# Kernel optimization log

Hardware: AMD Instinct MI355X
Metric: run time of the kernel (lower is better)

Reference implementation:

```python
import jax, jax.numpy as jnp
import numpy as np

B, N, D = 4, 4096, 1024
H, DH = 16, 64
EPS = 1e-5


def setup_inputs() -> dict:
    key = jax.random.key(0)
    ks = jax.random.split(key, 4)
    x = jax.random.normal(ks[0], (B, N, D), dtype=jnp.float32)
    w_qkv = jax.random.normal(ks[1], (D, 3 * H * DH), dtype=jnp.float32) * 0.02
    # per-head LayerNorm affine params (one LayerNorm(dim_head) per head)
    gamma_k = jnp.ones((H, DH), dtype=jnp.float32)
    beta_k = jnp.zeros((H, DH), dtype=jnp.float32)
    gamma_v = jnp.ones((H, DH), dtype=jnp.float32)
    beta_v = jnp.zeros((H, DH), dtype=jnp.float32)
    w_out = jax.random.normal(ks[2], (H * DH, D), dtype=jnp.float32) * 0.02
    b_out = jnp.zeros((D,), dtype=jnp.float32)
    return {"x": x, "w_qkv": w_qkv, "gamma_k": gamma_k, "beta_k": beta_k,
            "gamma_v": gamma_v, "beta_v": beta_v, "w_out": w_out, "b_out": b_out}


def _per_head_layernorm(t, gamma, beta):
    # t: [b, h, n, d]; gamma/beta: [h, d] (distinct affine per head)
    mu = jnp.mean(t, axis=-1, keepdims=True)
    var = jnp.mean(jnp.square(t - mu), axis=-1, keepdims=True)  # biased, as torch LayerNorm
    tn = (t - mu) * jax.lax.rsqrt(var + EPS)
    return tn * gamma[None, :, None, :] + beta[None, :, None, :]


def reference(x, w_qkv, gamma_k, beta_k, gamma_v, beta_v, w_out, b_out):
    b, n, _ = x.shape
    h, dh = gamma_k.shape
    qkv = jnp.einsum('bnd,de->bne', x, w_qkv)  # [b, n, 3*h*dh]
    q, k, v = jnp.split(qkv, 3, axis=-1)

    def to_heads(t):  # b n (h d) -> b h n d
        return t.reshape(b, n, h, dh).transpose(0, 2, 1, 3)

    q, k, v = to_heads(q), to_heads(k), to_heads(v)
    k = _per_head_layernorm(k, gamma_k, beta_k)
    v = _per_head_layernorm(v, gamma_v, beta_v)
    # linear attention: scores = k^T v / n  -> [b, h, d, d]
    scores = jnp.einsum('bhnd,bhne->bhde', k, v) / n
    out = jnp.einsum('bhnd,bhde->bhne', q, scores)  # [b, h, n, d]
    out = out.transpose(0, 2, 1, 3).reshape(b, n, h * dh)
    return jnp.einsum('bne,ed->bnd', out, w_out) + b_out
```

## Files before the change

kernel.cpp:

```cpp
#include <hip/hip_runtime.h>

typedef __attribute__((ext_vector_type(4))) float f32x4;
typedef __attribute__((ext_vector_type(8))) short s16x8;

#define DEV static __device__ __forceinline__

typedef __attribute__((address_space(3))) void lds_t;
typedef __attribute__((address_space(1))) void gbl_t;

DEV void gload_lds16(const void* g, void* l) {
    __builtin_amdgcn_global_load_lds((gbl_t*)g, (lds_t*)l, 16, 0, 0);
}

DEV ushort f2bf(float f) {
    unsigned u = __float_as_uint(f);
    u += 0x7fffu + ((u >> 16) & 1u);
    return (ushort)(u >> 16);
}
DEV float bf2f(ushort h) { return __uint_as_float(((unsigned)h) << 16); }

#define FULLBAR() do {                              \
    __builtin_amdgcn_sched_barrier(0);              \
    asm volatile("" ::: "memory");                  \
    __builtin_amdgcn_s_barrier();                   \
    asm volatile("" ::: "memory");                  \
    __builtin_amdgcn_sched_barrier(0);              \
} while (0)

#define WAITVM(n) asm volatile("s_waitcnt vmcnt(" #n ")" ::: "memory")
#define LGKM0() asm volatile("s_waitcnt lgkmcnt(0)" ::: "memory")

__global__ void pack_x_k(const float* __restrict__ x, ushort* __restrict__ xb, int n4) {
    int stride = gridDim.x * blockDim.x;
    for (int i = blockIdx.x * blockDim.x + threadIdx.x; i < n4; i += stride) {
        float4 v = reinterpret_cast<const float4*>(x)[i];
        ushort4 o;
        o.x = f2bf(v.x); o.y = f2bf(v.y); o.z = f2bf(v.z); o.w = f2bf(v.w);
        reinterpret_cast<ushort4*>(xb)[i] = o;
    }
}

__global__ void pack_wq_k(const float* __restrict__ w, ushort* __restrict__ o) {
    int i = blockIdx.x * 256 + threadIdx.x;
    int r = i >> 8, c4 = i & 255;
    float4 v = *reinterpret_cast<const float4*>(w + (size_t)r * 3072 + c4 * 4);
    ushort4 u;
    u.x = f2bf(v.x); u.y = f2bf(v.y); u.z = f2bf(v.z); u.w = f2bf(v.w);
    *reinterpret_cast<ushort4*>(o + (size_t)r * 1024 + c4 * 4) = u;
}

__global__ void trans_pack_k(const float* __restrict__ in, ushort* __restrict__ out,
                             int R, int C, int col0) {
    __shared__ float tile[32][33];
    int bx = col0 + blockIdx.x * 32, by = blockIdx.y * 32;
    int tx = threadIdx.x, ty = threadIdx.y;
#pragma unroll
    for (int i = 0; i < 32; i += 8)
        tile[ty + i][tx] = in[(size_t)(by + ty + i) * C + bx + tx];
    __syncthreads();
#pragma unroll
    for (int i = 0; i < 32; i += 8)
        out[(size_t)(bx - col0 + ty + i) * R + by + tx] = f2bf(tile[tx][ty + i]);
}

template <int MODE>
__global__ __launch_bounds__(512, 1) void gemm_bt_k(
    const ushort* __restrict__ A, const ushort* __restrict__ Bt,
    int Nn, int col0, size_t b_stride,
    ushort* __restrict__ ko, ushort* __restrict__ vo,
    const float* __restrict__ gk, const float* __restrict__ bk,
    const float* __restrict__ gv, const float* __restrict__ bv,
    const float* __restrict__ bias, float* __restrict__ outf)
{
    __shared__ __align__(16) ushort SH[65536];
    const int t = threadIdx.x;
    const int w = t >> 6, lane = t & 63;
    const int wr = w >> 2, wc = w & 3;
    const int lrow = lane & 15, kh = lane >> 4;

    int bid = blockIdx.y * gridDim.x + blockIdx.x;
    int C8 = (gridDim.x * gridDim.y) >> 3;
    int nid = (bid & 7) * C8 + (bid >> 3);
    int n0 = (nid % gridDim.x) * 256;
    int m0 = (nid / gridDim.x) * 256;

    const ushort* Bte = (MODE == 1) ? Bt + (size_t)(m0 >> 12) * b_stride : Bt;

    const int srow8 = w * 8 + (lane >> 3);
    const int scol = ((lane & 7) ^ ((lane >> 3) & 7)) * 8;

    const int g0 = ((kh) ^ (lrow & 7)) * 8;
    const int g1 = ((4 + kh) ^ (lrow & 7)) * 8;

    f32x4 acc[8][4] = {};
    s16x8 bfr[4][2];
    s16x8 af[8];

    auto STAGE_A = [&](int kt, int s, int h) {
        ushort* As = SH + s * 32768;
        const ushort* Ag = A + (size_t)(m0 + h * 128 + srow8) * 1024 + kt * 64 + scol;
        gload_lds16(Ag,                     As + (h * 128 + w * 8) * 64);
        gload_lds16(Ag + (size_t)64 * 1024, As + (h * 128 + 64 + w * 8) * 64);
    };
    auto STAGE_B = [&](int kt, int s, int h) {
        ushort* Bs = SH + s * 32768 + 16384;
        const ushort* Bg = Bte + (size_t)(n0 + h * 128 + srow8) * 1024 + kt * 64 + scol;
        gload_lds16(Bg,                     Bs + (h * 128 + w * 8) * 64);
        gload_lds16(Bg + (size_t)64 * 1024, Bs + (h * 128 + 64 + w * 8) * 64);
    };

    STAGE_A(0, 0, 0); STAGE_A(0, 0, 1);
    STAGE_B(0, 0, 0); STAGE_B(0, 0, 1);
    STAGE_B(1, 1, 0); STAGE_B(1, 1, 1);

    for (int kt = 0; kt < 16; ++kt) {
        const int p = kt & 1, q = p ^ 1;
        const ushort* As = SH + p * 32768;
        const ushort* Bs = As + 16384;

        if (kt < 15) { WAITVM(4); } else { WAITVM(0); }
        FULLBAR();

#pragma unroll
        for (int ni = 0; ni < 4; ni++) {
            const int r = (wc * 64 + ni * 16 + lrow) * 64;
            bfr[ni][0] = *reinterpret_cast<const s16x8*>(&Bs[r + g0]);
            bfr[ni][1] = *reinterpret_cast<const s16x8*>(&Bs[r + g1]);
        }
#pragma unroll
        for (int mi = 0; mi < 8; mi++)
            af[mi] = *reinterpret_cast<const s16x8*>(&As[(wr * 128 + mi * 16 + lrow) * 64 + g0]);
        if (kt + 1 < 16) { STAGE_A(kt + 1, q, 0); STAGE_A(kt + 1, q, 1); }

        __builtin_amdgcn_s_setprio(1);
#pragma unroll
        for (int mi = 0; mi < 8; mi++)
#pragma unroll
            for (int ni = 0; ni < 4; ni++)
                acc[mi][ni] = __builtin_amdgcn_mfma_f32_16x16x32_bf16(af[mi], bfr[ni][0], acc[mi][ni], 0, 0, 0);
        __builtin_amdgcn_s_setprio(0);

        LGKM0();
        FULLBAR();

        if (kt + 2 < 16) { STAGE_B(kt + 2, p, 0); STAGE_B(kt + 2, p, 1); }
#pragma unroll
        for (int mi = 0; mi < 8; mi++)
            af[mi] = *reinterpret_cast<const s16x8*>(&As[(wr * 128 + mi * 16 + lrow) * 64 + g1]);

        __builtin_amdgcn_s_setprio(1);
#pragma unroll
        for (int mi = 0; mi < 8; mi++)
#pragma unroll
            for (int ni = 0; ni < 4; ni++)
                acc[mi][ni] = __builtin_amdgcn_mfma_f32_16x16x32_bf16(af[mi], bfr[ni][1], acc[mi][ni], 0, 0, 0);
        __builtin_amdgcn_s_setprio(0);
    }

    if (MODE == 0) {
        const int e0 = col0 + n0 + wc * 64;
        const int which = e0 >> 10;
        const int h = (e0 >> 6) & 15;
        const float* g  = (which == 1) ? gk : gv;
        const float* bb = (which == 1) ? bk : bv;
        ushort* dst     = (which == 1) ? ko : vo;
        float gr[4], br[4];
#pragma unroll
        for (int ni = 0; ni < 4; ni++) {
            gr[ni] = g[h * 64 + ni * 16 + lrow];
            br[ni] = bb[h * 64 + ni * 16 + lrow];
        }
        __syncthreads();
        ushort* Tl = SH + w * 4608;
#pragma unroll
        for (int chunk = 0; chunk < 2; ++chunk) {
#pragma unroll
            for (int mi2 = 0; mi2 < 4; ++mi2) {
                const int mi = chunk * 4 + mi2;
#pragma unroll
                for (int j = 0; j < 4; j++) {
                    float s = acc[mi][0][j] + acc[mi][1][j] + acc[mi][2][j] + acc[mi][3][j];
                    s += __shfl_xor(s, 1, 64);
                    s += __shfl_xor(s, 2, 64);
                    s += __shfl_xor(s, 4, 64);
                    s += __shfl_xor(s, 8, 64);
                    float mu = s * (1.f / 64.f);
                    float t2 = 0.f;
#pragma unroll
                    for (int ni = 0; ni < 4; ni++) {
                        float dd = acc[mi][ni][j] - mu;
                        t2 += dd * dd;
                    }
                    t2 += __shfl_xor(t2, 1, 64);
                    t2 += __shfl_xor(t2, 2, 64);
                    t2 += __shfl_xor(t2, 4, 64);
                    t2 += __shfl_xor(t2, 8, 64);
                    float inv = rsqrtf(t2 * (1.f / 64.f) + 1e-5f);
#pragma unroll
                    for (int ni = 0; ni < 4; ni++) {
                        float y = (acc[mi][ni][j] - mu) * inv * gr[ni] + br[ni];
                        Tl[(ni * 16 + lrow) * 72 + mi2 * 16 + kh * 4 + j] = f2bf(y);
                    }
                }
            }
            const int mrow0 = m0 + wr * 128 + chunk * 64;
            const int b = mrow0 >> 12, ns0 = mrow0 & 4095;
            ushort* obase = dst + (((size_t)b * 16 + h) * 64) * 4096 + ns0;
#pragma unroll
            for (int p2 = 0; p2 < 8; ++p2) {
                int d = p2 * 8 + (lane >> 3);
                int mo = (lane & 7) * 8;
                s16x8 vv = *reinterpret_cast<const s16x8*>(&Tl[d * 72 + mo]);
                *reinterpret_cast<s16x8*>(obase + (size_t)d * 4096 + mo) = vv;
            }
        }
    } else {
#pragma unroll
        for (int mi = 0; mi < 8; mi++)
#pragma unroll
            for (int ni = 0; ni < 4; ni++) {
                int e = n0 + wc * 64 + ni * 16 + lrow;
                float bv2 = bias[e];
#pragma unroll
                for (int j = 0; j < 4; j++) {
                    int m = m0 + wr * 128 + mi * 16 + kh * 4 + j;
                    outf[(size_t)m * Nn + e] = acc[mi][ni][j] + bv2;
                }
            }
    }
}

__global__ __launch_bounds__(256) void fold_k(const ushort* __restrict__ A,
                                              const ushort* __restrict__ Bt,
                                              ushort* __restrict__ out)
{
    __shared__ __align__(16) ushort SH2[24576];
    const int t = threadIdx.x;
    const int w = t >> 6, lane = t & 63;
    const int wm = w >> 1, wn = w & 1;
    const int lrow = lane & 15, kh = lane >> 4;
    const int n0 = blockIdx.x * 128, m0 = blockIdx.y * 128;

    const int srow0 = w * 32 + (lane >> 2);
    const int scolSwz = (((lane & 3) ^ ((lane >> 3) & 3)) * 8);

    f32x4 acc[4][4] = {};

    auto STAGE = [&](int kt, int s) {
        ushort* As = SH2 + s * 8192;
        ushort* Bs = As + 4096;
        const ushort* Ag = A  + (size_t)(m0 + srow0) * 1024 + kt * 32 + scolSwz;
        const ushort* Bg = Bt + (size_t)(n0 + srow0) * 1024 + kt * 32 + scolSwz;
        gload_lds16(Ag,             As + w * 1024);
        gload_lds16(Bg,             Bs + w * 1024);
        gload_lds16(Ag + 16 * 1024, As + w * 1024 + 512);
        gload_lds16(Bg + 16 * 1024, Bs + w * 1024 + 512);
    };

    const int rdoff = (kh ^ ((lrow >> 1) & 3)) * 8;

    auto COMPUTE = [&](int s) {
        const ushort* As = SH2 + s * 8192;
        const ushort* Bs = As + 4096;
        s16x8 af[4], bfr[4];
#pragma unroll
        for (int mi = 0; mi < 4; mi++)
            af[mi] = *reinterpret_cast<const s16x8*>(&As[(wm * 64 + mi * 16 + lrow) * 32 + rdoff]);
#pragma unroll
        for (int ni = 0; ni < 4; ni++)
            bfr[ni] = *reinterpret_cast<const s16x8*>(&Bs[(wn * 64 + ni * 16 + lrow) * 32 + rdoff]);
#pragma unroll
        for (int mi = 0; mi < 4; mi++)
#pragma unroll
            for (int ni = 0; ni < 4; ni++)
                acc[mi][ni] = __builtin_amdgcn_mfma_f32_16x16x32_bf16(af[mi], bfr[ni], acc[mi][ni], 0, 0, 0);
    };

    STAGE(0, 0);
    STAGE(1, 1);
    int ss = 2, sc_ = 0;
    for (int kt = 0; kt < 30; ++kt) {
        STAGE(kt + 2, ss);
        ss = (ss == 2) ? 0 : ss + 1;
        WAITVM(8);
        FULLBAR();
        COMPUTE(sc_);
        sc_ = (sc_ == 2) ? 0 : sc_ + 1;
        FULLBAR();
    }
    WAITVM(4); FULLBAR(); COMPUTE(0); FULLBAR();
    WAITVM(0); FULLBAR(); COMPUTE(1);

#pragma unroll
    for (int mi = 0; mi < 4; mi++)
#pragma unroll
        for (int ni = 0; ni < 4; ni++) {
            int e = n0 + wn * 64 + ni * 16 + lrow;
#pragma unroll
            for (int j = 0; j < 4; j++) {
                int m = m0 + wm * 64 + mi * 16 + kh * 4 + j;
                out[(size_t)m * 1024 + e] = f2bf(acc[mi][ni][j]);
            }
        }
}

__global__ __launch_bounds__(256) void scores_k(const ushort* __restrict__ kT,
                                                const ushort* __restrict__ vT,
                                                float* __restrict__ sc)
{
    __shared__ float red[4][64][65];
    const int bh = blockIdx.y;
    const int t = threadIdx.x;
    const int w = t >> 6, lane = t & 63;
    const int lrow = lane & 15, kh = lane >> 4;
    const ushort* ka = kT + (size_t)bh * 64 * 4096;
    const ushort* va = vT + (size_t)bh * 64 * 4096;
    const int n0 = blockIdx.x * 512 + w * 128;

    f32x4 acc[4][4] = {};
#pragma unroll
    for (int ks = 0; ks < 4; ++ks) {
        const int n = n0 + ks * 32 + kh * 8;
        s16x8 af[4], bfr[4];
#pragma unroll
        for (int mi = 0; mi < 4; mi++)
            af[mi] = *reinterpret_cast<const s16x8*>(ka + (size_t)(mi * 16 + lrow) * 4096 + n);
#pragma unroll
        for (int ni = 0; ni < 4; ni++)
            bfr[ni] = *reinterpret_cast<const s16x8*>(va + (size_t)(ni * 16 + lrow) * 4096 + n);
#pragma unroll
        for (int mi = 0; mi < 4; mi++)
#pragma unroll
            for (int ni = 0; ni < 4; ni++)
                acc[mi][ni] = __builtin_amdgcn_mfma_f32_16x16x32_bf16(af[mi], bfr[ni], acc[mi][ni], 0, 0, 0);
    }
#pragma unroll
    for (int mi = 0; mi < 4; mi++)
#pragma unroll
        for (int ni = 0; ni < 4; ni++)
#pragma unroll
            for (int j = 0; j < 4; j++)
                red[w][mi * 16 + kh * 4 + j][ni * 16 + lrow] = acc[mi][ni][j];
    __syncthreads();
    const float scale = 1.f / 4096.f;
    for (int idx = t; idx < 4096; idx += 256) {
        int d = idx >> 6, e = idx & 63;
        float s = red[0][d][e] + red[1][d][e] + red[2][d][e] + red[3][d][e];
        atomicAdd(&sc[(size_t)bh * 4096 + idx], s * scale);
    }
}

__global__ __launch_bounds__(256) void wprime_k(const float* __restrict__ sc,
                                                const ushort* __restrict__ woutT,
                                                ushort* __restrict__ wpT)
{
    __shared__ float scl[64][65];
    __shared__ ushort wl[128][72];
    int bh = blockIdx.y;
    int b = bh >> 4, h = bh & 15;
    int f0 = blockIdx.x * 128;
    int t = threadIdx.x;
    for (int i = t; i < 4096; i += 256) {
        int d2 = i >> 6, e = i & 63;
        scl[e][d2] = sc[(size_t)bh * 4096 + i];
    }
    for (int i = t; i < 1024; i += 256) {
        int fl = i >> 3, c = i & 7;
        *reinterpret_cast<int4*>(&wl[fl][c * 8]) =
            *reinterpret_cast<const int4*>(woutT + (size_t)(f0 + fl) * 1024 + h * 64 + c * 8);
    }
    __syncthreads();
    int dd = (t & 7) * 8;
    int fl0 = t >> 3;
#pragma unroll
    for (int fi = 0; fi < 4; ++fi) {
        int fl = fi * 32 + fl0;
        float acc[8] = {};
        for (int e = 0; e < 64; ++e) {
            float wv = bf2f(wl[fl][e]);
#pragma unroll
            for (int i = 0; i < 8; ++i)
                acc[i] = fmaf(wv, scl[e][dd + i], acc[i]);
        }
        ushort4 o0, o1;
        o0.x = f2bf(acc[0]); o0.y = f2bf(acc[1]); o0.z = f2bf(acc[2]); o0.w = f2bf(acc[3]);
        o1.x = f2bf(acc[4]); o1.y = f2bf(acc[5]); o1.z = f2bf(acc[6]); o1.w = f2bf(acc[7]);
        ushort* op = wpT + ((size_t)b * 1024 + f0 + fl) * 1024 + h * 64 + dd;
        *reinterpret_cast<ushort4*>(op) = o0;
        *reinterpret_cast<ushort4*>(op + 4) = o1;
    }
}

extern "C" void kernel_launch(void* const* d_in, const int* in_sizes, int n_in,
                              void* d_out, int out_size, void* d_ws, size_t ws_size,
                              hipStream_t stream)
{
    const float* x       = (const float*)d_in[0];
    const float* w_qkv   = (const float*)d_in[1];
    const float* gamma_k = (const float*)d_in[2];
    const float* beta_k  = (const float*)d_in[3];
    const float* gamma_v = (const float*)d_in[4];
    const float* beta_v  = (const float*)d_in[5];
    const float* w_out   = (const float*)d_in[6];
    const float* b_out   = (const float*)d_in[7];
    float* out = (float*)d_out;

    char* ws = (char*)d_ws;
    const size_t MB = 1024 * 1024;
    ushort* xb    = (ushort*)(ws);
    ushort* wkvT  = (ushort*)(ws + 32 * MB);
    ushort* woutT = (ushort*)(ws + 38 * MB);
    ushort* wqb   = (ushort*)(ws + 40 * MB);
    ushort* kb    = (ushort*)(ws + 48 * MB);
    ushort* vb    = (ushort*)(ws + 80 * MB);
    float*  sc    = (float*)(ws + 112 * MB);
    ushort* wpT   = (ushort*)(ws + 120 * MB);
    ushort* fT    = (ushort*)(ws + 128 * MB);

    pack_x_k<<<2048, 256, 0, stream>>>(x, xb, 16384 * 1024 / 4);
    pack_wq_k<<<1024, 256, 0, stream>>>(w_qkv, wqb);
    trans_pack_k<<<dim3(64, 32), dim3(32, 8), 0, stream>>>(w_qkv, wkvT, 1024, 3072, 1024);
    trans_pack_k<<<dim3(32, 32), dim3(32, 8), 0, stream>>>(w_out, woutT, 1024, 1024, 0);
    gemm_bt_k<0><<<dim3(8, 64), 512, 0, stream>>>(xb, wkvT, 2048, 1024, 0,
                                                  kb, vb,
                                                  gamma_k, beta_k, gamma_v, beta_v,
                                                  nullptr, nullptr);
    hipMemsetAsync(sc, 0, 64 * 4096 * sizeof(float), stream);
    scores_k<<<dim3(8, 64), 256, 0, stream>>>(kb, vb, sc);
    wprime_k<<<dim3(8, 64), 256, 0, stream>>>(sc, woutT, wpT);
    fold_k<<<dim3(8, 32), 256, 0, stream>>>(wpT, wqb, fT);
    gemm_bt_k<1><<<dim3(4, 64), 512, 0, stream>>>(xb, fT, 1024, 0, (size_t)1048576,
                                                  nullptr, nullptr,
                                                  nullptr, nullptr, nullptr, nullptr,
                                                  b_out, out);
}
```

Measured before the change: 213.9 us.

## Fuse k^T v scores into KV projection GEMM epilogue, drop K/V buffers

Reorders the packed K/V weight columns so each 256-wide GEMM tile holds matching K and V heads. The GEMM epilogue then applies the per-head LayerNorm, stores normalized K and V in swizzled LDS, and computes the per-tile k^T v partial product with MFMA, accumulating it into the scores buffer with atomics. This removes the separate scores kernel and the 64 MB bf16 K/V round-trip through global memory. The cost is a longer epilogue and many more atomic adds, since each 256-row tile now contributes its own partial.

```diff
diff --git a/kernel.cpp b/kernel.cpp
--- a/kernel.cpp
+++ b/kernel.cpp
@@ -63,11 +63,28 @@
         out[(size_t)(bx - col0 + ty + i) * R + by + tx] = f2bf(tile[tx][ty + i]);
 }
 
+__global__ void trans_pack_kv(const float* __restrict__ in, ushort* __restrict__ out) {
+    __shared__ float tile[32][33];
+    int bxo = blockIdx.x * 32;
+    int by = blockIdx.y * 32;
+    int blk = bxo >> 8, grp = (bxo >> 6) & 3, d0 = bxo & 63;
+    int h = blk * 2 + (grp >> 1);
+    int src = 1024 + (grp & 1) * 1024 + h * 64 + d0;
+    int tx = threadIdx.x, ty = threadIdx.y;
+#pragma unroll
+    for (int i = 0; i < 32; i += 8)
+        tile[ty + i][tx] = in[(size_t)(by + ty + i) * 3072 + src + tx];
+    __syncthreads();
+#pragma unroll
+    for (int i = 0; i < 32; i += 8)
+        out[(size_t)(bxo + ty + i) * 1024 + by + tx] = f2bf(tile[tx][ty + i]);
+}
+
 template <int MODE>
 __global__ __launch_bounds__(512, 1) void gemm_bt_k(
     const ushort* __restrict__ A, const ushort* __restrict__ Bt,
-    int Nn, int col0, size_t b_stride,
-    ushort* __restrict__ ko, ushort* __restrict__ vo,
+    int Nn, size_t b_stride,
+    float* __restrict__ scp,
     const float* __restrict__ gk, const float* __restrict__ bk,
     const float* __restrict__ gv, const float* __restrict__ bv,
     const float* __restrict__ bias, float* __restrict__ outf)
@@ -158,12 +175,11 @@
     }
 
     if (MODE == 0) {
-        const int e0 = col0 + n0 + wc * 64;
-        const int which = e0 >> 10;
-        const int h = (e0 >> 6) & 15;
-        const float* g  = (which == 1) ? gk : gv;
-        const float* bb = (which == 1) ? bk : bv;
-        ushort* dst     = (which == 1) ? ko : vo;
+        const int i_nb = n0 >> 8;
+        const int h = i_nb * 2 + (wc >> 1);
+        const int is_k = ((wc & 1) == 0);
+        const float* g  = is_k ? gk : gv;
+        const float* bb = is_k ? bk : bv;
         float gr[4], br[4];
 #pragma unroll
         for (int ni = 0; ni < 4; ni++) {
@@ -171,49 +187,67 @@
             br[ni] = bb[h * 64 + ni * 16 + lrow];
         }
         __syncthreads();
-        ushort* Tl = SH + w * 4608;
-#pragma unroll
-        for (int chunk = 0; chunk < 2; ++chunk) {
-#pragma unroll
-            for (int mi2 = 0; mi2 < 4; ++mi2) {
-                const int mi = chunk * 4 + mi2;
-#pragma unroll
-                for (int j = 0; j < 4; j++) {
-                    float s = acc[mi][0][j] + acc[mi][1][j] + acc[mi][2][j] + acc[mi][3][j];
-                    s += __shfl_xor(s, 1, 64);
-                    s += __shfl_xor(s, 2, 64);
-                    s += __shfl_xor(s, 4, 64);
-                    s += __shfl_xor(s, 8, 64);
-                    float mu = s * (1.f / 64.f);
-                    float t2 = 0.f;
-#pragma unroll
-                    for (int ni = 0; ni < 4; ni++) {
-                        float dd = acc[mi][ni][j] - mu;
-                        t2 += dd * dd;
-                    }
-                    t2 += __shfl_xor(t2, 1, 64);
-                    t2 += __shfl_xor(t2, 2, 64);
-                    t2 += __shfl_xor(t2, 4, 64);
-                    t2 += __shfl_xor(t2, 8, 64);
-                    float inv = rsqrtf(t2 * (1.f / 64.f) + 1e-5f);
-#pragma unroll
-                    for (int ni = 0; ni < 4; ni++) {
-                        float y = (acc[mi][ni][j] - mu) * inv * gr[ni] + br[ni];
-                        Tl[(ni * 16 + lrow) * 72 + mi2 * 16 + kh * 4 + j] = f2bf(y);
-                    }
+        ushort* kvl = SH + wc * 16384;
+#pragma unroll
+        for (int mi = 0; mi < 8; mi++)
+#pragma unroll
+            for (int j = 0; j < 4; j++) {
+                float s = acc[mi][0][j] + acc[mi][1][j] + acc[mi][2][j] + acc[mi][3][j];
+                s += __shfl_xor(s, 1, 64);
+                s += __shfl_xor(s, 2, 64);
+                s += __shfl_xor(s, 4, 64);
+                s += __shfl_xor(s, 8, 64);
+                float mu = s * (1.f / 64.f);
+                float t2 = 0.f;
+#pragma unroll
+                for (int ni = 0; ni < 4; ni++) {
+                    float dd = acc[mi][ni][j] - mu;
+                    t2 += dd * dd;
+                }
+                t2 += __shfl_xor(t2, 1, 64);
+                t2 += __shfl_xor(t2, 2, 64);
+                t2 += __shfl_xor(t2, 4, 64);
+                t2 += __shfl_xor(t2, 8, 64);
+                float inv = rsqrtf(t2 * (1.f / 64.f) + 1e-5f);
+                const int n = wr * 128 + mi * 16 + kh * 4 + j;
+#pragma unroll
+                for (int ni = 0; ni < 4; ni++) {
+                    float y = (acc[mi][ni][j] - mu) * inv * gr[ni] + br[ni];
+                    const int c = ni * 16 + lrow;
+                    const int gn = (n >> 3) ^ (c & 31);
+                    kvl[c * 256 + gn * 8 + (n & 7)] = f2bf(y);
                 }
             }
-            const int mrow0 = m0 + wr * 128 + chunk * 64;
-            const int b = mrow0 >> 12, ns0 = mrow0 & 4095;
-            ushort* obase = dst + (((size_t)b * 16 + h) * 64) * 4096 + ns0;
-#pragma unroll
-            for (int p2 = 0; p2 < 8; ++p2) {
-                int d = p2 * 8 + (lane >> 3);
-                int mo = (lane & 7) * 8;
-                s16x8 vv = *reinterpret_cast<const s16x8*>(&Tl[d * 72 + mo]);
-                *reinterpret_cast<s16x8*>(obase + (size_t)d * 4096 + mo) = vv;
+        __syncthreads();
+        const int hp = w >> 2, T = w & 3;
+        const ushort* Ak = SH + (hp * 2) * 16384;
+        const ushort* Bv = SH + (hp * 2 + 1) * 16384;
+        const int arow = T * 16 + lrow;
+        f32x4 sacc[4] = {};
+#pragma unroll
+        for (int ks = 0; ks < 8; ++ks) {
+            const int gnr = ks * 4 + kh;
+            s16x8 afk = *reinterpret_cast<const s16x8*>(
+                &Ak[arow * 256 + ((gnr ^ (arow & 31)) * 8)]);
+#pragma unroll
+            for (int ni = 0; ni < 4; ni++) {
+                const int erow = ni * 16 + lrow;
+                s16x8 bfv = *reinterpret_cast<const s16x8*>(
+                    &Bv[erow * 256 + ((gnr ^ (erow & 31)) * 8)]);
+                sacc[ni] = __builtin_amdgcn_mfma_f32_16x16x32_bf16(afk, bfv, sacc[ni], 0, 0, 0);
             }
         }
+        const int bh = (m0 >> 12) * 16 + i_nb * 2 + hp;
+        float* scb = scp + (size_t)bh * 4096;
+        const float scale = 1.f / 4096.f;
+#pragma unroll
+        for (int ni = 0; ni < 4; ni++)
+#pragma unroll
+            for (int j = 0; j < 4; j++) {
+                const int d = T * 16 + kh * 4 + j;
+                const int e = ni * 16 + lrow;
+                atomicAdd(&scb[d * 64 + e], sacc[ni][j] * scale);
+            }
     } else {
 #pragma unroll
         for (int mi = 0; mi < 8; mi++)
@@ -302,52 +336,6 @@
                 out[(size_t)m * 1024 + e] = f2bf(acc[mi][ni][j]);
             }
         }
-}
-
-__global__ __launch_bounds__(256) void scores_k(const ushort* __restrict__ kT,
-                                                const ushort* __restrict__ vT,
-                                                float* __restrict__ sc)
-{
-    __shared__ float red[4][64][65];
-    const int bh = blockIdx.y;
-    const int t = threadIdx.x;
-    const int w = t >> 6, lane = t & 63;
-    const int lrow = lane & 15, kh = lane >> 4;
-    const ushort* ka = kT + (size_t)bh * 64 * 4096;
-    const ushort* va = vT + (size_t)bh * 64 * 4096;
-    const int n0 = blockIdx.x * 512 + w * 128;
-
-    f32x4 acc[4][4] = {};
-#pragma unroll
-    for (int ks = 0; ks < 4; ++ks) {
-        const int n = n0 + ks * 32 + kh * 8;
-        s16x8 af[4], bfr[4];
-#pragma unroll
-        for (int mi = 0; mi < 4; mi++)
-            af[mi] = *reinterpret_cast<const s16x8*>(ka + (size_t)(mi * 16 + lrow) * 4096 + n);
-#pragma unroll
-        for (int ni = 0; ni < 4; ni++)
-            bfr[ni] = *reinterpret_cast<const s16x8*>(va + (size_t)(ni * 16 + lrow) * 4096 + n);
-#pragma unroll
-        for (int mi = 0; mi < 4; mi++)
-#pragma unroll
-            for (int ni = 0; ni < 4; ni++)
-                acc[mi][ni] = __builtin_amdgcn_mfma_f32_16x16x32_bf16(af[mi], bfr[ni], acc[mi][ni], 0, 0, 0);
-    }
-#pragma unroll
-    for (int mi = 0; mi < 4; mi++)
-#pragma unroll
-        for (int ni = 0; ni < 4; ni++)
-#pragma unroll
-            for (int j = 0; j < 4; j++)
-                red[w][mi * 16 + kh * 4 + j][ni * 16 + lrow] = acc[mi][ni][j];
-    __syncthreads();
-    const float scale = 1.f / 4096.f;
-    for (int idx = t; idx < 4096; idx += 256) {
-        int d = idx >> 6, e = idx & 63;
-        float s = red[0][d][e] + red[1][d][e] + red[2][d][e] + red[3][d][e];
-        atomicAdd(&sc[(size_t)bh * 4096 + idx], s * scale);
-    }
 }
 
 __global__ __launch_bounds__(256) void wprime_k(const float* __restrict__ sc,
@@ -411,26 +399,23 @@
     ushort* wkvT  = (ushort*)(ws + 32 * MB);
     ushort* woutT = (ushort*)(ws + 38 * MB);
     ushort* wqb   = (ushort*)(ws + 40 * MB);
-    ushort* kb    = (ushort*)(ws + 48 * MB);
-    ushort* vb    = (ushort*)(ws + 80 * MB);
-    float*  sc    = (float*)(ws + 112 * MB);
-    ushort* wpT   = (ushort*)(ws + 120 * MB);
-    ushort* fT    = (ushort*)(ws + 128 * MB);
+    float*  sc    = (float*)(ws + 48 * MB);
+    ushort* wpT   = (ushort*)(ws + 56 * MB);
+    ushort* fT    = (ushort*)(ws + 64 * MB);
 
     pack_x_k<<<2048, 256, 0, stream>>>(x, xb, 16384 * 1024 / 4);
     pack_wq_k<<<1024, 256, 0, stream>>>(w_qkv, wqb);
-    trans_pack_k<<<dim3(64, 32), dim3(32, 8), 0, stream>>>(w_qkv, wkvT, 1024, 3072, 1024);
+    trans_pack_kv<<<dim3(64, 32), dim3(32, 8), 0, stream>>>(w_qkv, wkvT);
     trans_pack_k<<<dim3(32, 32), dim3(32, 8), 0, stream>>>(w_out, woutT, 1024, 1024, 0);
-    gemm_bt_k<0><<<dim3(8, 64), 512, 0, stream>>>(xb, wkvT, 2048, 1024, 0,
-                                                  kb, vb,
+    hipMemsetAsync(sc, 0, 64 * 4096 * sizeof(float), stream);
+    gemm_bt_k<0><<<dim3(8, 64), 512, 0, stream>>>(xb, wkvT, 2048, 0,
+                                                  sc,
                                                   gamma_k, beta_k, gamma_v, beta_v,
                                                   nullptr, nullptr);
-    hipMemsetAsync(sc, 0, 64 * 4096 * sizeof(float), stream);
-    scores_k<<<dim3(8, 64), 256, 0, stream>>>(kb, vb, sc);
     wprime_k<<<dim3(8, 64), 256, 0, stream>>>(sc, woutT, wpT);
     fold_k<<<dim3(8, 32), 256, 0, stream>>>(wpT, wqb, fT);
-    gemm_bt_k<1><<<dim3(4, 64), 512, 0, stream>>>(xb, fT, 1024, 0, (size_t)1048576,
-                                                  nullptr, nullptr,
+    gemm_bt_k<1><<<dim3(4, 64), 512, 0, stream>>>(xb, fT, 1024, (size_t)1048576,
+                                                  nullptr,
                                                   nullptr, nullptr, nullptr, nullptr,
                                                   b_out, out);
 }
```

After: 197.3 us. 1.08x faster.
